# Kernel optimization log

Hardware: AMD Instinct MI355X
Metric: run time of the kernel (lower is better)

The kernel has to match this reference:

```python
import jax, jax.numpy as jnp
import numpy as np

B, L, C, H, W = 2, 32, 128, 32, 32
R_MIN, R_MAX = 0.8, 0.99


def setup_inputs() -> dict:
    key = jax.random.key(0)
    ks = jax.random.split(key, 12)
    x = jax.random.normal(ks[0], (B, L, C, H, W), jnp.float32)
    # LRU initialization exactly as in the torch module
    u1 = jax.random.uniform(ks[1], (C, H), jnp.float32)
    u2 = jax.random.uniform(ks[2], (C, H), jnp.float32)
    nu_log = jnp.log(-0.5 * jnp.log(u1 * (R_MAX**2 - R_MIN**2) + R_MIN**2))
    theta_log = jnp.log(u2 * 2.0 * jnp.pi)
    abs_lam = jnp.exp(-jnp.exp(nu_log))  # |lambda| = exp(-nu)
    gamma_log = jnp.log(jnp.sqrt(1.0 - abs_lam**2))
    params_log = jnp.concatenate([nu_log, theta_log, gamma_log], axis=0)  # [3C, H]
    s = 0.05
    Wb_re = jax.random.normal(ks[3], (C, C), jnp.float32) * s
    Wb_im = jax.random.normal(ks[4], (C, C), jnp.float32) * s
    bb_re = jax.random.normal(ks[5], (C,), jnp.float32) * s
    bb_im = jax.random.normal(ks[6], (C,), jnp.float32) * s
    Wc_re = jax.random.normal(ks[7], (C, C), jnp.float32) * s
    Wc_im = jax.random.normal(ks[8], (C, C), jnp.float32) * s
    bc_re = jax.random.normal(ks[9], (C,), jnp.float32) * s
    bc_im = jax.random.normal(ks[10], (C,), jnp.float32) * s
    ln_w = jnp.ones((C, H, W), jnp.float32)
    ln_b = jnp.zeros((C, H, W), jnp.float32)
    return dict(x=x, params_log=params_log, Wb_re=Wb_re, Wb_im=Wb_im, bb_re=bb_re,
                bb_im=bb_im, Wc_re=Wc_re, Wc_im=Wc_im, bc_re=bc_re, bc_im=bc_im,
                ln_w=ln_w, ln_b=ln_b)


def reference(x, params_log, Wb_re, Wb_im, bb_re, bb_im, Wc_re, Wc_im, bc_re, bc_im, ln_w, ln_b):
    Cn = x.shape[2]
    nu = jnp.exp(params_log[:Cn])           # [C,H]
    theta = jnpp_exp = jnp.exp(params_log[Cn:2 * Cn])
    gamma = jnp.exp(params_log[2 * Cn:])    # [C,H]
    lam = jnp.exp(-nu + 1j * theta)         # [C,H] complex, |lam|<1

    # FFT2 over spatial dims
    h = jnp.fft.fft2(x.astype(jnp.complex64))  # [B,L,C,H,W]
    # complex 1x1 conv proj_B (CxC GEMM per pixel)
    Wb = (Wb_re + 1j * Wb_im).astype(jnp.complex64)
    bb = (bb_re + 1j * bb_im).astype(jnp.complex64)
    h = jnp.einsum('oc,blchw->blohw', Wb, h) + bb[None, None, :, None, None]
    # gamma gating, broadcast over B,L,W
    h = h * gamma[None, None, :, :, None]

    # linear recurrence y_t = lam * y_{t-1} + h_t (pscan), lam constant in t
    lam_b = lam[None, :, :, None]  # [1,C,H,1] broadcasts over [B,C,H,W]
    def step(carry, ht):
        y = lam_b * carry + ht
        return y, y
    h_t = jnp.moveaxis(h, 1, 0)  # [L,B,C,H,W]
    _, ys = jax.lax.scan(step, jnp.zeros_like(h_t[0]), h_t)
    h = jnp.moveaxis(ys, 0, 1)   # [B,L,C,H,W]
    last_hidden_out = h[:, -1:]

    h = jnp.fft.ifft2(h)
    Wc = (Wc_re + 1j * Wc_im).astype(jnp.complex64)
    bc = (bc_re + 1j * bc_im).astype(jnp.complex64)
    h = jnp.einsum('oc,blchw->blohw', Wc, h) + bc[None, None, :, None, None]
    h = h.real  # real cast, dropout is identity in eval

    # LayerNorm over (C,H,W) jointly
    mean = jnp.mean(h, axis=(2, 3, 4), keepdims=True)
    var = jnp.var(h, axis=(2, 3, 4), keepdims=True)
    h = (h - mean) / jnp.sqrt(var + 1e-5) * ln_w + ln_b
    return h + x, last_hidden_out
```

## Files before the change

kernel.cpp:

```cpp
#include <hip/hip_runtime.h>
#include <cstdint>
#include <cstddef>

#define DEVINL __device__ __forceinline__

static constexpr int Bdim = 2, Ldim = 32, Cdim = 128, Hdim = 32, Wdim = 32;
static constexpr int HW  = Hdim * Wdim;
static constexpr int CHW = Cdim * HW;
static constexpr size_t OUT0_ELEMS = (size_t)Bdim * Ldim * CHW;
static constexpr size_t OUT1_CPLX  = (size_t)Bdim * CHW;

typedef __attribute__((ext_vector_type(8))) short short8v;
typedef __attribute__((ext_vector_type(4))) float f32x4;

DEVINL int bitrev5(int v) {
    return ((v&1)<<4) | ((v&2)<<2) | (v&4) | ((v&8)>>2) | ((v&16)>>4);
}
DEVINL unsigned short f2bf(float v) {
    unsigned u = __float_as_uint(v);
    return (unsigned short)((u + 0x7FFFu + ((u >> 16) & 1u)) >> 16);
}
DEVINL void bfsplit(float v, short& hi, short& lo) {
    unsigned short hb = f2bf(v);
    hi = (short)hb;
    float hf = __uint_as_float(((unsigned)hb) << 16);
    lo = (short)f2bf(v - hf);
}
DEVINL unsigned pack2bf(float2 v) {
    return (unsigned)f2bf(v.x) | ((unsigned)f2bf(v.y) << 16);
}
DEVINL float2 unpack2bf(unsigned u) {
    return make_float2(__uint_as_float(u << 16), __uint_as_float(u & 0xFFFF0000u));
}

template<int INV>
DEVINL void fft32_reg(float2 v[32]) {
    constexpr float TC[16] = { 1.0f, 0.980785280f, 0.923879533f, 0.831469612f,
                               0.707106781f, 0.555570233f, 0.382683432f, 0.195090322f,
                               0.0f, -0.195090322f, -0.382683432f, -0.555570233f,
                              -0.707106781f, -0.831469612f, -0.923879533f, -0.980785280f };
    constexpr float TS[16] = { 0.0f, -0.195090322f, -0.382683432f, -0.555570233f,
                              -0.707106781f, -0.831469612f, -0.923879533f, -0.980785280f,
                              -1.0f, -0.980785280f, -0.923879533f, -0.831469612f,
                              -0.707106781f, -0.555570233f, -0.382683432f, -0.195090322f };
#pragma unroll
    for (int st = 0; st < 5; ++st) {
        const int half = 1 << st;
#pragma unroll
        for (int bf = 0; bf < 16; ++bf) {
            const int g = bf >> st;
            const int j = bf & (half - 1);
            const int i0 = (g << (st+1)) + j;
            const float wr = TC[j << (4-st)];
            const float wi = INV ? -TS[j << (4-st)] : TS[j << (4-st)];
            float2 a0 = v[i0], a1 = v[i0+half];
            float tr = wr*a1.x - wi*a1.y;
            float ti = wr*a1.y + wi*a1.x;
            v[i0]      = make_float2(a0.x+tr, a0.y+ti);
            v[i0+half] = make_float2(a0.x-tr, a0.y-ti);
        }
    }
}

__global__ __launch_bounds__(256) void fft_h_fwd_bf_kernel(const float* __restrict__ x,
                                                           unsigned* __restrict__ Hf) {
    const int gid = blockIdx.x*256 + threadIdx.x;
    const int w = gid & 31;
    const size_t slice = (size_t)(gid >> 5);
    const float* src = x + slice*HW + w;
    float2 v[32];
#pragma unroll
    for (int i = 0; i < 32; ++i)
        v[i] = make_float2(src[(size_t)bitrev5(i)*Wdim], 0.f);
    fft32_reg<0>(v);
    unsigned* dst = Hf + slice*HW + w;
#pragma unroll
    for (int h = 0; h < 32; ++h) dst[(size_t)h*Wdim] = pack2bf(v[h]);
}

__global__ __launch_bounds__(256) void ifft_h_bf_kernel(const unsigned* __restrict__ Sin,
                                                        unsigned* __restrict__ Ysp) {
    const int gid = blockIdx.x*256 + threadIdx.x;
    const int w = gid & 31;
    const size_t slice = (size_t)(gid >> 5);
    const unsigned* src = Sin + slice*HW + w;
    float2 v[32];
#pragma unroll
    for (int i = 0; i < 32; ++i)
        v[i] = unpack2bf(src[(size_t)bitrev5(i)*Wdim]);
    fft32_reg<1>(v);
    const float sc = 1.0f / 32.0f;
    unsigned* dst = Ysp + slice*HW + w;
#pragma unroll
    for (int h = 0; h < 32; ++h)
        dst[(size_t)h*Wdim] = pack2bf(make_float2(v[h].x*sc, v[h].y*sc));
}

template<int CPLX>
__global__ __launch_bounds__(256) void fft_w_out1_kernel(const float2* __restrict__ st31,
                                                         float* __restrict__ out1) {
    const int row = blockIdx.x*256 + threadIdx.x;
    const float2* src = st31 + (size_t)row*32;
    float2 v[32];
#pragma unroll
    for (int i = 0; i < 32; ++i) v[i] = src[bitrev5(i)];
    fft32_reg<0>(v);
    if (CPLX) {
        float2* dst = reinterpret_cast<float2*>(out1) + (size_t)row*32;
#pragma unroll
        for (int i = 0; i < 32; ++i) dst[i] = v[i];
    } else {
        float* dst = out1 + (size_t)row*32;
#pragma unroll
        for (int i = 0; i < 32; ++i) dst[i] = v[i].x;
    }
}

__global__ __launch_bounds__(256) void pack_w_kernel(
    const float* __restrict__ Wb_re, const float* __restrict__ Wb_im,
    const float* __restrict__ Wc_re, const float* __restrict__ Wc_im,
    short* __restrict__ Apack)
{
    const int gid = blockIdx.x*256 + threadIdx.x;
    const int a    = gid >> 12;
    const int rem  = gid & 4095;
    const int f    = rem >> 6;
    const int lane = rem & 63;
    const int m  = f >> 3, kc = f & 7;
    const int row = m*16 + (lane & 15);
    const int kbase = kc*32 + ((lane >> 4) << 3);
    short8v hi8, lo8;
#pragma unroll
    for (int j = 0; j < 8; ++j) {
        const int k = kbase + j;
        const int half = k >> 7;
        const int c = k & 127;
        float v;
        if (a == 0)      v = half ? -Wb_im[row*Cdim + c] : Wb_re[row*Cdim + c];
        else if (a == 1) v = half ?  Wb_re[row*Cdim + c] : Wb_im[row*Cdim + c];
        else             v = half ? -Wc_im[row*Cdim + c] : Wc_re[row*Cdim + c];
        short h, l; bfsplit(v, h, l);
        hi8[j] = h; lo8[j] = l;
    }
    const size_t off = (size_t)(f*64 + lane)*8;
    *reinterpret_cast<short8v*>(Apack + (size_t)(2*a)  *32768 + off) = hi8;
    *reinterpret_cast<short8v*>(Apack + (size_t)(2*a+1)*32768 + off) = lo8;
}

template<int MODE>
__global__ __launch_bounds__(256) void mix_mfma3_kernel(
    const unsigned* __restrict__ Yin,
    unsigned* __restrict__ Sout,
    const short* __restrict__ Apack,
    const float* __restrict__ bre, const float* __restrict__ bim,
    const float* __restrict__ pl,
    unsigned short* __restrict__ outr,
    float2* __restrict__ lnpart)
{
    __shared__ short Bs[8][4][64][8];
    const int bx = blockIdx.x;
    const int bl = bx >> 4, tt = bx & 15;
    const int t = threadIdx.x;
    const int wv = t >> 6, lane = t & 63;

    const unsigned* src = Yin + (size_t)bl*CHW + tt*64;
#pragma unroll
    for (int g = 0; g < 4; ++g) {
        const int id = g*256 + t;
        const int hw = id & 63;
        const int co = id >> 6;
        const int kc = co >> 2;
        const int ln = (co & 3)*16 + (hw & 15);
        const int nt4 = hw >> 4;
        unsigned u[8];
#pragma unroll
        for (int j = 0; j < 8; ++j)
            u[j] = src[(size_t)(co*8 + j)*HW + hw];
        unsigned re[4], im[4];
#pragma unroll
        for (int p = 0; p < 4; ++p) {
            re[p] = (u[2*p] & 0xFFFFu) | (u[2*p+1] << 16);
            im[p] = (u[2*p] >> 16) | (u[2*p+1] & 0xFFFF0000u);
        }
        *reinterpret_cast<uint4*>(&Bs[kc][nt4][ln][0])   = make_uint4(re[0], re[1], re[2], re[3]);
        *reinterpret_cast<uint4*>(&Bs[kc+4][nt4][ln][0]) = make_uint4(im[0], im[1], im[2], im[3]);
    }
    __syncthreads();

    f32x4 accRe[2][4];
    f32x4 accIm[2][4];
#pragma unroll
    for (int mi = 0; mi < 2; ++mi)
#pragma unroll
        for (int nt = 0; nt < 4; ++nt) {
            accRe[mi][nt] = (f32x4)(0.0f);
            accIm[mi][nt] = (f32x4)(0.0f);
        }

    const short* Are_hi = Apack + (MODE == 0 ? 0 : 4)*32768;
    const short* Are_lo = Are_hi + 32768;
    const short* Aim_hi = Apack + 2*32768;
    const short* Aim_lo = Aim_hi + 32768;

#pragma unroll 2
    for (int kc = 0; kc < 8; ++kc) {
        short8v bh[4];
#pragma unroll
        for (int nt = 0; nt < 4; ++nt)
            bh[nt] = *reinterpret_cast<const short8v*>(&Bs[kc][nt][lane][0]);
#pragma unroll
        for (int mi = 0; mi < 2; ++mi) {
            const int m = wv*2 + mi;
            const size_t off = (size_t)((m*8 + kc)*64 + lane)*8;
            const short8v arh = *reinterpret_cast<const short8v*>(Are_hi + off);
            const short8v arl = *reinterpret_cast<const short8v*>(Are_lo + off);
#pragma unroll
            for (int nt = 0; nt < 4; ++nt) {
                accRe[mi][nt] = __builtin_amdgcn_mfma_f32_16x16x32_bf16(arh, bh[nt], accRe[mi][nt], 0, 0, 0);
                accRe[mi][nt] = __builtin_amdgcn_mfma_f32_16x16x32_bf16(arl, bh[nt], accRe[mi][nt], 0, 0, 0);
            }
            if (MODE == 0) {
                const short8v aih = *reinterpret_cast<const short8v*>(Aim_hi + off);
                const short8v ail = *reinterpret_cast<const short8v*>(Aim_lo + off);
#pragma unroll
                for (int nt = 0; nt < 4; ++nt) {
                    accIm[mi][nt] = __builtin_amdgcn_mfma_f32_16x16x32_bf16(aih, bh[nt], accIm[mi][nt], 0, 0, 0);
                    accIm[mi][nt] = __builtin_amdgcn_mfma_f32_16x16x32_bf16(ail, bh[nt], accIm[mi][nt], 0, 0, 0);
                }
            }
        }
    }

    const int col   = lane & 15;
    const int rbase = (lane >> 4) * 4;
    float lns = 0.f, lnq = 0.f;
#pragma unroll
    for (int mi = 0; mi < 2; ++mi) {
#pragma unroll
        for (int r = 0; r < 4; ++r) {
            const int o = wv*32 + mi*16 + rbase + r;
            if (MODE == 0) {
                const float br = bre[o], bi = bim[o];
                const float g0 = expf(pl[(2*Cdim + o)*Hdim + 2*tt]);
                const float g1 = expf(pl[(2*Cdim + o)*Hdim + 2*tt + 1]);
#pragma unroll
                for (int nt = 0; nt < 4; ++nt) {
                    const int wcol = nt*16 + col;
                    const float g = (nt < 2) ? g0 : g1;
                    const float bsel = ((wcol & 31) == 0) ? 1.0f : 0.0f;
                    float2 rv;
                    rv.x = (accRe[mi][nt][r] + br*bsel) * g;
                    rv.y = (accIm[mi][nt][r] + bi*bsel) * g;
                    Sout[(size_t)bl*CHW + (size_t)o*HW + tt*64 + wcol] = pack2bf(rv);
                }
            } else {
                const float br = bre[o];
#pragma unroll
                for (int nt = 0; nt < 4; ++nt) {
                    const int wcol = nt*16 + col;
                    const float v = accRe[mi][nt][r] + br;
                    outr[(size_t)bl*CHW + (size_t)o*HW + tt*64 + wcol] = f2bf(v);
                    lns += v; lnq += v*v;
                }
            }
        }
    }
    if (MODE == 1) {
#pragma unroll
        for (int off = 32; off > 0; off >>= 1) {
            lns += __shfl_down(lns, off);
            lnq += __shfl_down(lnq, off);
        }
        __shared__ float2 red[4];
        if (lane == 0) red[wv] = make_float2(lns, lnq);
        __syncthreads();
        if (t == 0) {
            float2 a = red[0], b2 = red[1], c2 = red[2], d = red[3];
            lnpart[bx] = make_float2(a.x + b2.x + c2.x + d.x, a.y + b2.y + c2.y + d.y);
        }
    }
}

__global__ __launch_bounds__(256) void scan_kernel(
    unsigned* __restrict__ Hf2, const float* __restrict__ pl, float2* __restrict__ st31)
{
    const int idx = blockIdx.x*256 + threadIdx.x;
    const int b   = idx >> 17;
    const int chw = idx & (CHW - 1);
    const int c   = chw >> 10;
    const int h   = (chw >> 5) & 31;
    const float nu = expf(pl[c*Hdim + h]);
    const float th = expf(pl[(Cdim + c)*Hdim + h]);
    const float rr = expf(-nu);
    const float lr = rr * cosf(th);
    const float li = rr * sinf(th);
    float2 y = make_float2(0.f, 0.f);
    const size_t basei = (size_t)b * Ldim * CHW + chw;
#pragma unroll 4
    for (int l = 0; l < Ldim; ++l) {
        float2 hv = unpack2bf(Hf2[basei + (size_t)l*CHW]);
        float yr = fmaf(lr, y.x, fmaf(-li, y.y, hv.x));
        float yi = fmaf(lr, y.y, fmaf( li, y.x, hv.y));
        y = make_float2(yr, yi);
        Hf2[basei + (size_t)l*CHW] = pack2bf(y);
    }
    st31[(size_t)b*CHW + chw] = y;
}

__global__ __launch_bounds__(64) void ln_finish_kernel(const float2* __restrict__ lnpart,
                                                       float2* __restrict__ stats) {
    const int bl = blockIdx.x;
    const int t = threadIdx.x;
    float s = 0.f, sq = 0.f;
    if (t < 16) { float2 v = lnpart[bl*16 + t]; s = v.x; sq = v.y; }
#pragma unroll
    for (int off = 8; off > 0; off >>= 1) {
        s  += __shfl_down(s, off);
        sq += __shfl_down(sq, off);
    }
    if (t == 0) {
        const float invN = 1.0f / (float)CHW;
        float mean = s * invN;
        float var  = sq * invN - mean*mean;
        stats[bl] = make_float2(mean, rsqrtf(var + 1e-5f));
    }
}

__global__ __launch_bounds__(256) void ln_apply_kernel(
    float* __restrict__ out0, const unsigned short* __restrict__ hpre,
    const float* __restrict__ x,
    const float* __restrict__ lnw, const float* __restrict__ lnb,
    const float2* __restrict__ stats)
{
    const int idx4 = blockIdx.x*256 + threadIdx.x;
    const int i = idx4 * 4;
    const int bl = i >> 17;
    const int chw4 = (i & (CHW - 1)) >> 2;
    const float2 st = stats[bl];
    const uint2 hu = reinterpret_cast<const uint2*>(hpre)[idx4];
    float4 h;
    h.x = __uint_as_float(hu.x << 16);
    h.y = __uint_as_float(hu.x & 0xFFFF0000u);
    h.z = __uint_as_float(hu.y << 16);
    h.w = __uint_as_float(hu.y & 0xFFFF0000u);
    float4 xv = reinterpret_cast<const float4*>(x)[idx4];
    float4 w  = reinterpret_cast<const float4*>(lnw)[chw4];
    float4 bb = reinterpret_cast<const float4*>(lnb)[chw4];
    const float m = st.x, rs = st.y;
    float4 r;
    r.x = fmaf((h.x - m)*rs, w.x, bb.x) + xv.x;
    r.y = fmaf((h.y - m)*rs, w.y, bb.y) + xv.y;
    r.z = fmaf((h.z - m)*rs, w.z, bb.z) + xv.z;
    r.w = fmaf((h.w - m)*rs, w.w, bb.w) + xv.w;
    reinterpret_cast<float4*>(out0)[idx4] = r;
}

extern "C" void kernel_launch(void* const* d_in, const int* in_sizes, int n_in,
                              void* d_out, int out_size, void* d_ws, size_t ws_size,
                              hipStream_t stream)
{
    const float* x     = (const float*)d_in[0];
    const float* pl    = (const float*)d_in[1];
    const float* Wb_re = (const float*)d_in[2];
    const float* Wb_im = (const float*)d_in[3];
    const float* bb_re = (const float*)d_in[4];
    const float* bb_im = (const float*)d_in[5];
    const float* Wc_re = (const float*)d_in[6];
    const float* Wc_im = (const float*)d_in[7];
    const float* bc_re = (const float*)d_in[8];
    const float* bc_im = (const float*)d_in[9];
    const float* ln_w  = (const float*)d_in[10];
    const float* ln_b  = (const float*)d_in[11];

    float* out0 = (float*)d_out;
    float* out1 = out0 + OUT0_ELEMS;

    char* ws = (char*)d_ws;
    unsigned*       bufA    = (unsigned*)       ws;
    unsigned*       bufB    = (unsigned*)       (ws + 33554432);
    unsigned short* out0pre = (unsigned short*) (ws + 67108864);
    float2*         st31    = (float2*)         (ws + 83886080);
    short*          Apack   = (short*)          (ws + 85983232);
    float2*         lnpart  = (float2*)         (ws + 86376448);
    float2*         stats   = (float2*)         (ws + 86384640);

    const bool interleaved = ((size_t)out_size >= OUT0_ELEMS + 2*OUT1_CPLX);

    pack_w_kernel<<<48, 256, 0, stream>>>(Wb_re, Wb_im, Wc_re, Wc_im, Apack);
    fft_h_fwd_bf_kernel<<<1024, 256, 0, stream>>>(x, bufA);
    mix_mfma3_kernel<0><<<1024, 256, 0, stream>>>(bufA, bufB, Apack, bb_re, bb_im, pl, nullptr, nullptr);
    scan_kernel<<<1024, 256, 0, stream>>>(bufB, pl, st31);
    if (interleaved)
        fft_w_out1_kernel<1><<<32, 256, 0, stream>>>(st31, out1);
    else
        fft_w_out1_kernel<0><<<32, 256, 0, stream>>>(st31, out1);
    ifft_h_bf_kernel<<<1024, 256, 0, stream>>>(bufB, bufA);
    mix_mfma3_kernel<1><<<1024, 256, 0, stream>>>(bufA, nullptr, Apack, bc_re, bc_im, pl, out0pre, lnpart);
    ln_finish_kernel<<<64, 64, 0, stream>>>(lnpart, stats);
    ln_apply_kernel<<<8192, 256, 0, stream>>>(out0, out0pre, x, ln_w, ln_b, stats);
}
```

Before: 107.4 us.

## Fuse inverse H-FFT into output mix and W-FFT into scan epilogue

The W-direction FFT of the last hidden state now runs inside the scan kernel through wave shuffles, which removes the st31 buffer and a separate launch. The inverse H-FFT is folded into the output channel-mix kernel: each block loads two W columns for all channels into LDS, runs the FFT in registers, writes bf16 B tiles into shared memory, and then does the MFMA GEMM. This drops a full bf16 round trip through global memory and one launch. In exchange, output stores are strided (two w per row), the block needs more LDS, and the block-to-XCD mapping changes.

```diff
diff --git a/kernel.cpp b/kernel.cpp
--- a/kernel.cpp
+++ b/kernel.cpp
@@ -78,44 +78,6 @@
     for (int h = 0; h < 32; ++h) dst[(size_t)h*Wdim] = pack2bf(v[h]);
 }
 
-__global__ __launch_bounds__(256) void ifft_h_bf_kernel(const unsigned* __restrict__ Sin,
-                                                        unsigned* __restrict__ Ysp) {
-    const int gid = blockIdx.x*256 + threadIdx.x;
-    const int w = gid & 31;
-    const size_t slice = (size_t)(gid >> 5);
-    const unsigned* src = Sin + slice*HW + w;
-    float2 v[32];
-#pragma unroll
-    for (int i = 0; i < 32; ++i)
-        v[i] = unpack2bf(src[(size_t)bitrev5(i)*Wdim]);
-    fft32_reg<1>(v);
-    const float sc = 1.0f / 32.0f;
-    unsigned* dst = Ysp + slice*HW + w;
-#pragma unroll
-    for (int h = 0; h < 32; ++h)
-        dst[(size_t)h*Wdim] = pack2bf(make_float2(v[h].x*sc, v[h].y*sc));
-}
-
-template<int CPLX>
-__global__ __launch_bounds__(256) void fft_w_out1_kernel(const float2* __restrict__ st31,
-                                                         float* __restrict__ out1) {
-    const int row = blockIdx.x*256 + threadIdx.x;
-    const float2* src = st31 + (size_t)row*32;
-    float2 v[32];
-#pragma unroll
-    for (int i = 0; i < 32; ++i) v[i] = src[bitrev5(i)];
-    fft32_reg<0>(v);
-    if (CPLX) {
-        float2* dst = reinterpret_cast<float2*>(out1) + (size_t)row*32;
-#pragma unroll
-        for (int i = 0; i < 32; ++i) dst[i] = v[i];
-    } else {
-        float* dst = out1 + (size_t)row*32;
-#pragma unroll
-        for (int i = 0; i < 32; ++i) dst[i] = v[i].x;
-    }
-}
-
 __global__ __launch_bounds__(256) void pack_w_kernel(
     const float* __restrict__ Wb_re, const float* __restrict__ Wb_im,
     const float* __restrict__ Wc_re, const float* __restrict__ Wc_im,
@@ -153,9 +115,7 @@
     unsigned* __restrict__ Sout,
     const short* __restrict__ Apack,
     const float* __restrict__ bre, const float* __restrict__ bim,
-    const float* __restrict__ pl,
-    unsigned short* __restrict__ outr,
-    float2* __restrict__ lnpart)
+    const float* __restrict__ pl)
 {
     __shared__ short Bs[8][4][64][8];
     const int bx = blockIdx.x;
@@ -233,56 +193,31 @@
 
     const int col   = lane & 15;
     const int rbase = (lane >> 4) * 4;
-    float lns = 0.f, lnq = 0.f;
 #pragma unroll
     for (int mi = 0; mi < 2; ++mi) {
 #pragma unroll
         for (int r = 0; r < 4; ++r) {
             const int o = wv*32 + mi*16 + rbase + r;
-            if (MODE == 0) {
-                const float br = bre[o], bi = bim[o];
-                const float g0 = expf(pl[(2*Cdim + o)*Hdim + 2*tt]);
-                const float g1 = expf(pl[(2*Cdim + o)*Hdim + 2*tt + 1]);
-#pragma unroll
-                for (int nt = 0; nt < 4; ++nt) {
-                    const int wcol = nt*16 + col;
-                    const float g = (nt < 2) ? g0 : g1;
-                    const float bsel = ((wcol & 31) == 0) ? 1.0f : 0.0f;
-                    float2 rv;
-                    rv.x = (accRe[mi][nt][r] + br*bsel) * g;
-                    rv.y = (accIm[mi][nt][r] + bi*bsel) * g;
-                    Sout[(size_t)bl*CHW + (size_t)o*HW + tt*64 + wcol] = pack2bf(rv);
-                }
-            } else {
-                const float br = bre[o];
-#pragma unroll
-                for (int nt = 0; nt < 4; ++nt) {
-                    const int wcol = nt*16 + col;
-                    const float v = accRe[mi][nt][r] + br;
-                    outr[(size_t)bl*CHW + (size_t)o*HW + tt*64 + wcol] = f2bf(v);
-                    lns += v; lnq += v*v;
-                }
+            const float br = bre[o], bi = bim[o];
+            const float g0 = expf(pl[(2*Cdim + o)*Hdim + 2*tt]);
+            const float g1 = expf(pl[(2*Cdim + o)*Hdim + 2*tt + 1]);
+#pragma unroll
+            for (int nt = 0; nt < 4; ++nt) {
+                const int wcol = nt*16 + col;
+                const float g = (nt < 2) ? g0 : g1;
+                const float bsel = ((wcol & 31) == 0) ? 1.0f : 0.0f;
+                float2 rv;
+                rv.x = (accRe[mi][nt][r] + br*bsel) * g;
+                rv.y = (accIm[mi][nt][r] + bi*bsel) * g;
+                Sout[(size_t)bl*CHW + (size_t)o*HW + tt*64 + wcol] = pack2bf(rv);
             }
         }
     }
-    if (MODE == 1) {
-#pragma unroll
-        for (int off = 32; off > 0; off >>= 1) {
-            lns += __shfl_down(lns, off);
-            lnq += __shfl_down(lnq, off);
-        }
-        __shared__ float2 red[4];
-        if (lane == 0) red[wv] = make_float2(lns, lnq);
-        __syncthreads();
-        if (t == 0) {
-            float2 a = red[0], b2 = red[1], c2 = red[2], d = red[3];
-            lnpart[bx] = make_float2(a.x + b2.x + c2.x + d.x, a.y + b2.y + c2.y + d.y);
-        }
-    }
-}
-
-__global__ __launch_bounds__(256) void scan_kernel(
-    unsigned* __restrict__ Hf2, const float* __restrict__ pl, float2* __restrict__ st31)
+}
+
+template<int CPLX>
+__global__ __launch_bounds__(256) void scan_fftw_kernel(
+    unsigned* __restrict__ Hf2, const float* __restrict__ pl, float* __restrict__ out1)
 {
     const int idx = blockIdx.x*256 + threadIdx.x;
     const int b   = idx >> 17;
@@ -304,7 +239,156 @@
         y = make_float2(yr, yi);
         Hf2[basei + (size_t)l*CHW] = pack2bf(y);
     }
-    st31[(size_t)b*CHW + chw] = y;
+    const int a = threadIdx.x & 31;
+    float2 v;
+    v.x = __shfl(y.x, bitrev5(a), 32);
+    v.y = __shfl(y.y, bitrev5(a), 32);
+#pragma unroll
+    for (int st = 0; st < 5; ++st) {
+        const int half = 1 << st;
+        const int j = a & (half - 1);
+        const float ang = -6.283185307179586f * (float)(j << (4 - st)) / 32.0f;
+        float wi, wr;
+        __sincosf(ang, &wi, &wr);
+        float2 p;
+        p.x = __shfl_xor(v.x, half, 32);
+        p.y = __shfl_xor(v.y, half, 32);
+        const bool top = (a & half) == 0;
+        const float2 a1 = top ? p : v;
+        const float2 a0 = top ? v : p;
+        const float tr = wr*a1.x - wi*a1.y;
+        const float ti = wr*a1.y + wi*a1.x;
+        v.x = top ? a0.x + tr : a0.x - tr;
+        v.y = top ? a0.y + ti : a0.y - ti;
+    }
+    const size_t row = (size_t)(idx >> 5);
+    if (CPLX) {
+        reinterpret_cast<float2*>(out1)[row*32 + a] = v;
+    } else {
+        out1[row*32 + a] = v.x;
+    }
+}
+
+__global__ __launch_bounds__(256) void mix_ifft_kernel(
+    const unsigned* __restrict__ Sin,
+    const short* __restrict__ Apack,
+    const float* __restrict__ bre,
+    unsigned short* __restrict__ outr,
+    float2* __restrict__ lnpart)
+{
+    __shared__ char smem[33792];
+    unsigned (*Sld)[2][33] = reinterpret_cast<unsigned(*)[2][33]>(smem);
+    short (*Bs)[4][64][8]  = reinterpret_cast<short(*)[4][64][8]>(smem);
+
+    const int bx  = blockIdx.x;
+    const int xcd = bx & 7;
+    const int q   = bx >> 3;
+    const int gg  = q >> 4;
+    const int wp  = q & 15;
+    const int bl  = xcd + 8*gg;
+    const int w0  = wp*2;
+    const int t   = threadIdx.x;
+    const int wv  = t >> 6, lane = t & 63;
+
+    const unsigned* src = Sin + (size_t)bl*CHW + w0;
+#pragma unroll
+    for (int it = 0; it < 16; ++it) {
+        const int id = it*256 + t;
+        const int c2 = id >> 5, hf = id & 31;
+        const unsigned* p = src + (size_t)c2*HW + hf*Wdim;
+        Sld[c2][0][hf] = p[0];
+        Sld[c2][1][hf] = p[1];
+    }
+    __syncthreads();
+
+    const int c  = t >> 1;
+    const int ws = t & 1;
+    float2 v[32];
+#pragma unroll
+    for (int i = 0; i < 32; ++i) v[i] = unpack2bf(Sld[c][ws][bitrev5(i)]);
+    fft32_reg<1>(v);
+    const float sc = 1.0f / 32.0f;
+#pragma unroll
+    for (int i = 0; i < 32; ++i) { v[i].x *= sc; v[i].y *= sc; }
+    __syncthreads();
+
+    {
+        const int kcr = c >> 5, kci = 4 + (c >> 5);
+        const int lnb = ((c >> 3) & 3) * 16;
+        const int j = c & 7;
+#pragma unroll
+        for (int h = 0; h < 32; ++h) {
+            const int n = ws*32 + h;
+            const int nt4 = n >> 4;
+            const int ln = lnb + (n & 15);
+            Bs[kcr][nt4][ln][j] = (short)f2bf(v[h].x);
+            Bs[kci][nt4][ln][j] = (short)f2bf(v[h].y);
+        }
+    }
+    __syncthreads();
+
+    f32x4 acc[2][4];
+#pragma unroll
+    for (int mi = 0; mi < 2; ++mi)
+#pragma unroll
+        for (int nt = 0; nt < 4; ++nt) acc[mi][nt] = (f32x4)(0.0f);
+
+    const short* A_hi = Apack + 4*32768;
+    const short* A_lo = A_hi + 32768;
+
+#pragma unroll 2
+    for (int kc = 0; kc < 8; ++kc) {
+        short8v bh[4];
+#pragma unroll
+        for (int nt = 0; nt < 4; ++nt)
+            bh[nt] = *reinterpret_cast<const short8v*>(&Bs[kc][nt][lane][0]);
+#pragma unroll
+        for (int mi = 0; mi < 2; ++mi) {
+            const int m = wv*2 + mi;
+            const size_t off = (size_t)((m*8 + kc)*64 + lane)*8;
+            const short8v arh = *reinterpret_cast<const short8v*>(A_hi + off);
+            const short8v arl = *reinterpret_cast<const short8v*>(A_lo + off);
+#pragma unroll
+            for (int nt = 0; nt < 4; ++nt) {
+                acc[mi][nt] = __builtin_amdgcn_mfma_f32_16x16x32_bf16(arh, bh[nt], acc[mi][nt], 0, 0, 0);
+                acc[mi][nt] = __builtin_amdgcn_mfma_f32_16x16x32_bf16(arl, bh[nt], acc[mi][nt], 0, 0, 0);
+            }
+        }
+    }
+
+    const int col   = lane & 15;
+    const int rbase = (lane >> 4) * 4;
+    float lns = 0.f, lnq = 0.f;
+#pragma unroll
+    for (int mi = 0; mi < 2; ++mi) {
+#pragma unroll
+        for (int r = 0; r < 4; ++r) {
+            const int o = wv*32 + mi*16 + rbase + r;
+            const float br = bre[o];
+#pragma unroll
+            for (int nt = 0; nt < 4; ++nt) {
+                const int n = nt*16 + col;
+                const int ws_o = n >> 5;
+                const int hh = n & 31;
+                const float val = acc[mi][nt][r] + br;
+                outr[(size_t)bl*CHW + (size_t)o*HW + (size_t)hh*Wdim + w0 + ws_o] = f2bf(val);
+                lns += val; lnq += val*val;
+            }
+        }
+    }
+#pragma unroll
+    for (int off = 32; off > 0; off >>= 1) {
+        lns += __shfl_down(lns, off);
+        lnq += __shfl_down(lnq, off);
+    }
+    __shared__ float2 red[4];
+    if (lane == 0) red[wv] = make_float2(lns, lnq);
+    __syncthreads();
+    if (t == 0) {
+        float2 a = red[0], b2 = red[1], c2 = red[2], d = red[3];
+        lnpart[bl*16 + wp] = make_float2(a.x + b2.x + c2.x + d.x,
+                                         a.y + b2.y + c2.y + d.y);
+    }
 }
 
 __global__ __launch_bounds__(64) void ln_finish_kernel(const float2* __restrict__ lnpart,
@@ -371,6 +455,7 @@
     const float* bc_im = (const float*)d_in[9];
     const float* ln_w  = (const float*)d_in[10];
     const float* ln_b  = (const float*)d_in[11];
+    (void)bc_im;
 
     float* out0 = (float*)d_out;
     float* out1 = out0 + OUT0_ELEMS;
@@ -379,23 +464,20 @@
     unsigned*       bufA    = (unsigned*)       ws;
     unsigned*       bufB    = (unsigned*)       (ws + 33554432);
     unsigned short* out0pre = (unsigned short*) (ws + 67108864);
-    float2*         st31    = (float2*)         (ws + 83886080);
-    short*          Apack   = (short*)          (ws + 85983232);
-    float2*         lnpart  = (float2*)         (ws + 86376448);
-    float2*         stats   = (float2*)         (ws + 86384640);
+    short*          Apack   = (short*)          (ws + 83886080);
+    float2*         lnpart  = (float2*)         (ws + 84279296);
+    float2*         stats   = (float2*)         (ws + 84287488);
 
     const bool interleaved = ((size_t)out_size >= OUT0_ELEMS + 2*OUT1_CPLX);
 
     pack_w_kernel<<<48, 256, 0, stream>>>(Wb_re, Wb_im, Wc_re, Wc_im, Apack);
     fft_h_fwd_bf_kernel<<<1024, 256, 0, stream>>>(x, bufA);
-    mix_mfma3_kernel<0><<<1024, 256, 0, stream>>>(bufA, bufB, Apack, bb_re, bb_im, pl, nullptr, nullptr);
-    scan_kernel<<<1024, 256, 0, stream>>>(bufB, pl, st31);
+    mix_mfma3_kernel<0><<<1024, 256, 0, stream>>>(bufA, bufB, Apack, bb_re, bb_im, pl);
     if (interleaved)
-        fft_w_out1_kernel<1><<<32, 256, 0, stream>>>(st31, out1);
+        scan_fftw_kernel<1><<<1024, 256, 0, stream>>>(bufB, pl, out1);
     else
-        fft_w_out1_kernel<0><<<32, 256, 0, stream>>>(st31, out1);
-    ifft_h_bf_kernel<<<1024, 256, 0, stream>>>(bufB, bufA);
-    mix_mfma3_kernel<1><<<1024, 256, 0, stream>>>(bufA, nullptr, Apack, bc_re, bc_im, pl, out0pre, lnpart);
+        scan_fftw_kernel<0><<<1024, 256, 0, stream>>>(bufB, pl, out1);
+    mix_ifft_kernel<<<1024, 256, 0, stream>>>(bufB, Apack, bc_re, out0pre, lnpart);
     ln_finish_kernel<<<64, 64, 0, stream>>>(lnpart, stats);
     ln_apply_kernel<<<8192, 256, 0, stream>>>(out0, out0pre, x, ln_w, ln_b, stats);
 }
```

After: 121.4 us. 13.1% more time.
